# Optimization experiments

Hardware: AMD Instinct MI355X
Metric: run time of the kernel (lower is better)

## Reference

```python
import jax, jax.numpy as jnp
import numpy as np

A, B, I, H, O = 400, 64, 50, 192, 3   # num_agents, batch, input_dim, hidden_dim, output_dim
ADIM, NH = 128, 8                      # attention_dim, num_heads
HD = ADIM // NH
SCALE = HD ** -0.5
EPS = 1e-5


def _ln(x, g, b):
    mu = jnp.mean(x, -1, keepdims=True)
    v = jnp.mean((x - mu) ** 2, -1, keepdims=True)
    return (x - mu) * jax.lax.rsqrt(v + EPS) * g + b


def setup_inputs() -> dict:
    key = jax.random.key(0)
    ks = jax.random.split(key, 12)
    s = 0.05
    n = lambda k, shape: (jax.random.normal(k, shape, jnp.float32) * s)
    return {
        'x': jax.random.normal(ks[0], (B, I), jnp.float32),
        'ln_in_g': jnp.ones((A, I), jnp.float32), 'ln_in_b': jnp.zeros((A, I), jnp.float32),
        'W1': n(ks[1], (A, I, H)), 'b1': jnp.zeros((A, H), jnp.float32),
        'Ws1': n(ks[2], (A, I, H)), 'bs1': jnp.zeros((A, H), jnp.float32),
        'W2': n(ks[3], (A, H, H)), 'b2': jnp.zeros((A, H), jnp.float32),
        'Ws2': n(ks[4], (A, H, H)), 'bs2': jnp.zeros((A, H), jnp.float32),
        'W3': n(ks[5], (A, H, H)), 'b3': jnp.zeros((A, H), jnp.float32),
        'ln_h_g': jnp.ones((A, H), jnp.float32), 'ln_h_b': jnp.zeros((A, H), jnp.float32),
        'Wout': n(ks[6], (A, H, O)), 'bout': jnp.zeros((A, O), jnp.float32),
        'aln_g': jnp.ones((H,), jnp.float32), 'aln_b': jnp.zeros((H,), jnp.float32),
        'Wq': n(ks[7], (H, ADIM)), 'bq': jnp.zeros((ADIM,), jnp.float32),
        'Wk': n(ks[8], (H, ADIM)), 'bk': jnp.zeros((ADIM,), jnp.float32),
        'Wv': n(ks[9], (H, ADIM)), 'bv': jnp.zeros((ADIM,), jnp.float32),
        'Wo': n(ks[10], (ADIM, H)), 'bo': jnp.zeros((H,), jnp.float32),
    }


def _forward(x, ln_in_g, ln_in_b, W1, b1, Ws1, bs1, W2, b2, Ws2, bs2, W3, b3,
             ln_h_g, ln_h_b, Wout, bout, aln_g, aln_b, Wq, bq, Wk, bk, Wv, bv, Wo, bo):
    gelu = lambda t: jax.nn.gelu(t, approximate=False)  # torch F.gelu default = exact erf
    # per-agent input LayerNorm (shared stats, per-agent affine) -> [A, B, I]
    xn = _ln(x[None, :, :], ln_in_g[:, None, :], ln_in_b[:, None, :])
    # agent MLPs as batched GEMMs over agent axis
    h1 = gelu(jnp.einsum('abi,aih->abh', xn, W1) + b1[:, None, :]) \
         + jnp.einsum('abi,aih->abh', xn, Ws1) + bs1[:, None, :]
    h2 = gelu(jnp.einsum('abh,ahk->abk', h1, W2) + b2[:, None, :]) \
         + jnp.einsum('abh,ahk->abk', h1, Ws2) + bs2[:, None, :]
    h3 = _ln(h2 + jnp.einsum('abh,ahk->abk', h2, W3) + b3[:, None, :],
             ln_h_g[:, None, :], ln_h_b[:, None, :])  # [A, B, H]
    # cross-SREK attention across the agent axis
    y = _ln(h3, aln_g, aln_b)
    q = (y @ Wq + bq).reshape(A, B, NH, HD).transpose(1, 2, 0, 3)  # [B, NH, A, HD]
    k = (y @ Wk + bk).reshape(A, B, NH, HD).transpose(1, 2, 0, 3)
    v = (y @ Wv + bv).reshape(A, B, NH, HD).transpose(1, 2, 0, 3)
    attn = jax.nn.softmax(jnp.einsum('bhad,bhcd->bhac', q, k) * SCALE, axis=-1)
    o = jnp.einsum('bhac,bhcd->bhad', attn, v).transpose(2, 0, 1, 3).reshape(A, B, ADIM)
    attended = h3 + (o @ Wo + bo)  # residual (dropout off in eval)
    # per-agent output heads -> [A, B, O]
    logits = jnp.einsum('abh,aho->abo', attended, Wout) + bout[:, None, :]
    return logits


def reference(x, ln_in_g, ln_in_b, W1, b1, Ws1, bs1, W2, b2, Ws2, bs2, W3, b3,
              ln_h_g, ln_h_b, Wout, bout, aln_g, aln_b, Wq, bq, Wk, bk, Wv, bv, Wo, bo):
    return _forward(x, ln_in_g, ln_in_b, W1, b1, Ws1, bs1, W2, b2, Ws2, bs2, W3, b3,
                    ln_h_g, ln_h_b, Wout, bout, aln_g, aln_b, Wq, bq, Wk, bk, Wv, bv, Wo, bo)
```

## Files before the change

### kernel.cpp

```cpp
#include <hip/hip_runtime.h>
#include <math.h>

#define AGENTS 400
#define BATCH  64
#define IDIM   50
#define HDIM   192
#define ODIM   3
#define ADIMM  128
#define NHEADS 8
#define HEADD  16
#define LN_EPS 1e-5f

#define PA   200
#define POUT 136

typedef __bf16 bf16x8 __attribute__((ext_vector_type(8)));
typedef float  f32x4  __attribute__((ext_vector_type(4)));

__device__ __forceinline__ float gelu_exact(float x) {
    return 0.5f * x * (1.0f + erff(x * 0.70710678118654752f));
}

__device__ __forceinline__ unsigned pack_bf16x2(float a, float b) {
    unsigned short ua = __builtin_bit_cast(unsigned short, (__bf16)a);
    unsigned short ub = __builtin_bit_cast(unsigned short, (__bf16)b);
    return (unsigned)ua | ((unsigned)ub << 16);
}

template<int NC, int KD, int NT, int NRG, int LDW, int PITCH>
__device__ __forceinline__ void gemm_bpass(f32x4 (&acc)[NRG][NT],
                                           const float* const* wptr,
                                           const __bf16* Asrc, int lane)
{
    const int r = lane & 15, g = lane >> 4;
    float buf[2][NT * 8];

    #pragma unroll
    for (int t = 0; t < NT; t++)
        #pragma unroll
        for (int j = 0; j < 8; j++) {
            int k = g * 8 + j;
            buf[0][t * 8 + j] = (k < KD) ? wptr[t][k * LDW + r] : 0.f;
        }

    #pragma unroll
    for (int c = 0; c < NC; c++) {
        const int cur = c & 1, nxt = cur ^ 1;
        if (c + 1 < NC) {
            #pragma unroll
            for (int t = 0; t < NT; t++)
                #pragma unroll
                for (int j = 0; j < 8; j++) {
                    int k = (c + 1) * 32 + g * 8 + j;
                    buf[nxt][t * 8 + j] = (k < KD) ? wptr[t][k * LDW + r] : 0.f;
                }
        }
        bf16x8 bfr[NT];
        #pragma unroll
        for (int t = 0; t < NT; t++)
            #pragma unroll
            for (int j = 0; j < 8; j++)
                bfr[t][j] = (__bf16)buf[cur][t * 8 + j];
        #pragma unroll
        for (int rg = 0; rg < NRG; rg++) {
            bf16x8 af = *(const bf16x8*)&Asrc[(16 * rg + r) * PITCH + c * 32 + g * 8];
            #pragma unroll
            for (int t = 0; t < NT; t++)
                acc[rg][t] = __builtin_amdgcn_mfma_f32_16x16x32_bf16(af, bfr[t], acc[rg][t], 0, 0, 0);
        }
    }
}

__global__ __launch_bounds__(512, 4) void mlp_kernel(
    const float* __restrict__ x,
    const float* __restrict__ ln_in_g, const float* __restrict__ ln_in_b,
    const float* __restrict__ W1, const float* __restrict__ b1,
    const float* __restrict__ Ws1, const float* __restrict__ bs1,
    const float* __restrict__ W2, const float* __restrict__ b2,
    const float* __restrict__ Ws2, const float* __restrict__ bs2,
    const float* __restrict__ W3, const float* __restrict__ b3,
    const float* __restrict__ ln_h_g, const float* __restrict__ ln_h_b,
    float* __restrict__ h3out)
{
    const int a    = blockIdx.x;
    const int tid  = threadIdx.x;
    const int wave = tid >> 6, lane = tid & 63;
    const int r = lane & 15, g = lane >> 4;
    const int cg = wave & 3, mh = wave >> 2;
    const int n0 = 48 * cg;
    const __bf16* Aw;

    __shared__ __align__(16) __bf16 As[64 * PA];
    __shared__ float mu_s[64], rs_s[64];
    Aw = As + 32 * mh * PA;

    {
        int rr = tid >> 3, l = tid & 7;
        float s = 0.f, ss = 0.f;
        for (int k = l; k < IDIM; k += 8) { float v = x[rr * IDIM + k]; s += v; ss += v * v; }
        #pragma unroll
        for (int off = 4; off; off >>= 1) {
            s  += __shfl_down(s,  off, 8);
            ss += __shfl_down(ss, off, 8);
        }
        if (l == 0) {
            float mu = s * (1.0f / IDIM);
            float var = ss * (1.0f / IDIM) - mu * mu;
            mu_s[rr] = mu;
            rs_s[rr] = rsqrtf(var + LN_EPS);
        }
    }
    __syncthreads();
    for (int sidx = tid; sidx < 64 * 64; sidx += 512) {
        int rr = sidx >> 6, k = sidx & 63;
        float v = 0.f;
        if (k < IDIM)
            v = (x[rr * IDIM + k] - mu_s[rr]) * rs_s[rr] * ln_in_g[a * IDIM + k] + ln_in_b[a * IDIM + k];
        As[rr * PA + k] = (__bf16)v;
    }
    __syncthreads();

    {
        const float* W1p  = W1  + (size_t)a * IDIM * HDIM;
        const float* Ws1p = Ws1 + (size_t)a * IDIM * HDIM;
        const float* wA[3] = { W1p + n0,  W1p + n0 + 16,  W1p + n0 + 32 };
        const float* wB[3] = { Ws1p + n0, Ws1p + n0 + 16, Ws1p + n0 + 32 };
        f32x4 acc1[2][3];
        #pragma unroll
        for (int i = 0; i < 2; i++)
            #pragma unroll
            for (int t = 0; t < 3; t++) acc1[i][t] = (f32x4)0.f;
        gemm_bpass<2, IDIM, 3, 2, HDIM, PA>(acc1, wA, Aw, lane);
        f32x4 acc2[2][3];
        #pragma unroll
        for (int i = 0; i < 2; i++)
            #pragma unroll
            for (int t = 0; t < 3; t++) acc2[i][t] = (f32x4)0.f;
        gemm_bpass<2, IDIM, 3, 2, HDIM, PA>(acc2, wB, Aw, lane);
        __syncthreads();
        #pragma unroll
        for (int t = 0; t < 3; t++) {
            int col = n0 + 16 * t + r;
            float bb  = b1[a * HDIM + col];
            float bbs = bs1[a * HDIM + col];
            #pragma unroll
            for (int rg = 0; rg < 2; rg++)
                #pragma unroll
                for (int i = 0; i < 4; i++) {
                    int row = 32 * mh + 16 * rg + 4 * g + i;
                    float v = gelu_exact(acc1[rg][t][i] + bb) + acc2[rg][t][i] + bbs;
                    As[row * PA + col] = (__bf16)v;
                }
        }
        __syncthreads();
    }

    {
        const float* W2p  = W2  + (size_t)a * HDIM * HDIM;
        const float* Ws2p = Ws2 + (size_t)a * HDIM * HDIM;
        const float* wA[3] = { W2p + n0,  W2p + n0 + 16,  W2p + n0 + 32 };
        const float* wB[3] = { Ws2p + n0, Ws2p + n0 + 16, Ws2p + n0 + 32 };
        f32x4 acc1[2][3];
        #pragma unroll
        for (int i = 0; i < 2; i++)
            #pragma unroll
            for (int t = 0; t < 3; t++) acc1[i][t] = (f32x4)0.f;
        gemm_bpass<6, HDIM, 3, 2, HDIM, PA>(acc1, wA, Aw, lane);
        f32x4 acc2[2][3];
        #pragma unroll
        for (int i = 0; i < 2; i++)
            #pragma unroll
            for (int t = 0; t < 3; t++) acc2[i][t] = (f32x4)0.f;
        gemm_bpass<6, HDIM, 3, 2, HDIM, PA>(acc2, wB, Aw, lane);
        __syncthreads();
        #pragma unroll
        for (int t = 0; t < 3; t++) {
            int col = n0 + 16 * t + r;
            float bb  = b2[a * HDIM + col];
            float bbs = bs2[a * HDIM + col];
            #pragma unroll
            for (int rg = 0; rg < 2; rg++)
                #pragma unroll
                for (int i = 0; i < 4; i++) {
                    int row = 32 * mh + 16 * rg + 4 * g + i;
                    float v = gelu_exact(acc1[rg][t][i] + bb) + acc2[rg][t][i] + bbs;
                    As[row * PA + col] = (__bf16)v;
                }
        }
        __syncthreads();
    }

    {
        const float* W3p = W3 + (size_t)a * HDIM * HDIM;
        const float* wA[3] = { W3p + n0, W3p + n0 + 16, W3p + n0 + 32 };
        f32x4 acc[2][3];
        #pragma unroll
        for (int i = 0; i < 2; i++)
            #pragma unroll
            for (int t = 0; t < 3; t++) acc[i][t] = (f32x4)0.f;
        gemm_bpass<6, HDIM, 3, 2, HDIM, PA>(acc, wA, Aw, lane);
        __syncthreads();
        #pragma unroll
        for (int t = 0; t < 3; t++) {
            int col = n0 + 16 * t + r;
            float bb = b3[a * HDIM + col];
            #pragma unroll
            for (int rg = 0; rg < 2; rg++)
                #pragma unroll
                for (int i = 0; i < 4; i++) {
                    int row = 32 * mh + 16 * rg + 4 * g + i;
                    float v = (float)As[row * PA + col] + acc[rg][t][i] + bb;
                    As[row * PA + col] = (__bf16)v;
                }
        }
        __syncthreads();
    }

    {
        int rr = tid >> 3, l = tid & 7;
        float s = 0.f, ss = 0.f;
        for (int k = l; k < HDIM; k += 8) { float v = (float)As[rr * PA + k]; s += v; ss += v * v; }
        #pragma unroll
        for (int off = 4; off; off >>= 1) {
            s  += __shfl_down(s,  off, 8);
            ss += __shfl_down(ss, off, 8);
        }
        if (l == 0) {
            float mu = s * (1.0f / HDIM);
            float var = ss * (1.0f / HDIM) - mu * mu;
            mu_s[rr] = mu;
            rs_s[rr] = rsqrtf(var + LN_EPS);
        }
    }
    __syncthreads();
    for (int sidx = tid; sidx < 64 * HDIM; sidx += 512) {
        int rr = sidx / HDIM, c = sidx - rr * HDIM;
        float v = ((float)As[rr * PA + c] - mu_s[rr]) * rs_s[rr] * ln_h_g[a * HDIM + c] + ln_h_b[a * HDIM + c];
        h3out[((size_t)a * BATCH + rr) * HDIM + c] = v;
    }
}

__global__ __launch_bounds__(512, 4) void qkv_kernel(
    const float* __restrict__ h3,
    const float* __restrict__ aln_g, const float* __restrict__ aln_b,
    const float* __restrict__ Wq, const float* __restrict__ bq,
    const float* __restrict__ Wk, const float* __restrict__ bk,
    const float* __restrict__ Wv, const float* __restrict__ bv,
    float* __restrict__ qT, float* __restrict__ kT, float* __restrict__ vT)
{
    const int a    = blockIdx.x;
    const int tid  = threadIdx.x;
    const int wave = tid >> 6, lane = tid & 63;
    const int r = lane & 15, g = lane >> 4;
    const int cg = wave & 3, mh = wave >> 2;

    __shared__ __align__(16) __bf16 ys[64 * PA];
    __shared__ float mu_s[64], rs_s[64];
    const __bf16* Aw = ys + 32 * mh * PA;

    {
        int rr = tid >> 3, l = tid & 7;
        const float* hp = h3 + ((size_t)a * BATCH + rr) * HDIM;
        float s = 0.f, ss = 0.f;
        for (int k = l; k < HDIM; k += 8) { float v = hp[k]; s += v; ss += v * v; }
        #pragma unroll
        for (int off = 4; off; off >>= 1) {
            s  += __shfl_down(s,  off, 8);
            ss += __shfl_down(ss, off, 8);
        }
        if (l == 0) {
            float mu = s * (1.0f / HDIM);
            float var = ss * (1.0f / HDIM) - mu * mu;
            mu_s[rr] = mu;
            rs_s[rr] = rsqrtf(var + LN_EPS);
        }
    }
    __syncthreads();
    for (int sidx = tid; sidx < 64 * HDIM; sidx += 512) {
        int rr = sidx / HDIM, c = sidx - rr * HDIM;
        float v = (h3[((size_t)a * BATCH + rr) * HDIM + c] - mu_s[rr]) * rs_s[rr] * aln_g[c] + aln_b[c];
        ys[rr * PA + c] = (__bf16)v;
    }
    __syncthreads();

    #pragma unroll
    for (int p = 0; p < 2; p++) {
        const int nb = 192 * p + 48 * cg;
        const float* wA[3];
        #pragma unroll
        for (int t = 0; t < 3; t++) {
            int nt = nb + 16 * t;
            const float* base = (nt < 128) ? Wq : (nt < 256) ? Wk : Wv;
            wA[t] = base + (nt & 127);
        }
        f32x4 acc[2][3];
        #pragma unroll
        for (int i = 0; i < 2; i++)
            #pragma unroll
            for (int t = 0; t < 3; t++) acc[i][t] = (f32x4)0.f;
        gemm_bpass<6, HDIM, 3, 2, ADIMM, PA>(acc, wA, Aw, lane);

        #pragma unroll
        for (int t = 0; t < 3; t++) {
            int n = nb + 16 * t + r;
            int which = n >> 7, cc = n & 127, hh = cc >> 4, dd = cc & 15;
            const float* bp = (which == 0) ? bq : (which == 1) ? bk : bv;
            float* op = (which == 0) ? qT : (which == 1) ? kT : vT;
            float bb = bp[cc];
            #pragma unroll
            for (int rg = 0; rg < 2; rg++)
                #pragma unroll
                for (int i = 0; i < 4; i++) {
                    int brow = 32 * mh + 16 * rg + 4 * g + i;
                    op[(((size_t)brow * NHEADS + hh) * AGENTS + a) * HEADD + dd] = acc[rg][t][i] + bb;
                }
        }
    }
}

#define PKA 24
#define PVA 408
#define PPA 232

__global__ __launch_bounds__(256, 2) void attn_kernel(
    const float* __restrict__ qT, const float* __restrict__ kT,
    const float* __restrict__ vT, float* __restrict__ oT)
{
    const int bh   = blockIdx.x;
    const int b    = bh >> 3, h = bh & 7;
    const int tid  = threadIdx.x;
    const int wave = tid >> 6, lane = tid & 63;
    const int r = lane & 15, g = lane >> 4;

    __shared__ __align__(16) __bf16 Ks[AGENTS * PKA];
    __shared__ __align__(16) __bf16 Vt[16 * PVA];
    __shared__ __align__(16) __bf16 Ps[4][16 * PPA];

    const float* kp = kT + (size_t)bh * AGENTS * HEADD;
    const float* vp = vT + (size_t)bh * AGENTS * HEADD;
    for (int idx = tid; idx < AGENTS * HEADD; idx += 256) {
        int a_ = idx >> 4, d = idx & 15;
        Ks[a_ * PKA + d] = (__bf16)kp[idx];
        Vt[d * PVA + a_] = (__bf16)vp[idx];
    }
    __bf16* Pw = Ps[wave];
    for (int z = lane; z < 16 * 16; z += 64)
        Pw[(z >> 4) * PPA + 208 + (z & 15)] = (__bf16)0.f;
    __syncthreads();

    for (int mt = wave; mt < 25; mt += 4) {
        const int m0 = mt * 16;

        bf16x8 aq;
        if (g < 2) {
            const float* qp = qT + ((size_t)bh * AGENTS + m0 + r) * HEADD + g * 8;
            #pragma unroll
            for (int j = 0; j < 8; j++) aq[j] = (__bf16)(qp[j] * 0.25f);
        } else {
            #pragma unroll
            for (int j = 0; j < 8; j++) aq[j] = (__bf16)0.f;
        }

        f32x4 sacc[25];
        #pragma unroll
        for (int t = 0; t < 25; t++) {
            bf16x8 bk_ = *(const bf16x8*)&Ks[(t * 16 + r) * PKA + (g & 1) * 8];
            sacc[t] = __builtin_amdgcn_mfma_f32_16x16x32_bf16(aq, bk_, (f32x4)0.f, 0, 0, 0);
        }

        float lv[4];
        #pragma unroll
        for (int i = 0; i < 4; i++) {
            float m_ = sacc[0][i];
            #pragma unroll
            for (int t = 1; t < 25; t++) m_ = fmaxf(m_, sacc[t][i]);
            #pragma unroll
            for (int off = 8; off; off >>= 1) m_ = fmaxf(m_, __shfl_xor(m_, off, 16));
            float l_ = 0.f;
            #pragma unroll
            for (int t = 0; t < 25; t++) {
                float p = __expf(sacc[t][i] - m_);
                sacc[t][i] = p;
                l_ += p;
            }
            #pragma unroll
            for (int off = 8; off; off >>= 1) l_ += __shfl_xor(l_, off, 16);
            lv[i] = l_;
        }

        f32x4 oacc = (f32x4)0.f;

        #pragma unroll
        for (int t = 0; t < 13; t++)
            #pragma unroll
            for (int i = 0; i < 4; i++)
                Pw[(g * 4 + i) * PPA + t * 16 + r] = (__bf16)sacc[t][i];
        __asm__ volatile("s_waitcnt lgkmcnt(0)" ::: "memory");
        #pragma unroll
        for (int c = 0; c < 7; c++) {
            bf16x8 ap  = *(const bf16x8*)&Pw[r * PPA + c * 32 + g * 8];
            bf16x8 bv_ = *(const bf16x8*)&Vt[r * PVA + c * 32 + g * 8];
            oacc = __builtin_amdgcn_mfma_f32_16x16x32_bf16(ap, bv_, oacc, 0, 0, 0);
        }

        for (int z = lane; z < 16 * 16; z += 64)
            Pw[(z >> 4) * PPA + 192 + (z & 15)] = (__bf16)0.f;
        #pragma unroll
        for (int t = 13; t < 25; t++)
            #pragma unroll
            for (int i = 0; i < 4; i++)
                Pw[(g * 4 + i) * PPA + (t - 13) * 16 + r] = (__bf16)sacc[t][i];
        __asm__ volatile("s_waitcnt lgkmcnt(0)" ::: "memory");
        #pragma unroll
        for (int c = 0; c < 6; c++) {
            bf16x8 ap  = *(const bf16x8*)&Pw[r * PPA + c * 32 + g * 8];
            bf16x8 bv_ = *(const bf16x8*)&Vt[r * PVA + 208 + c * 32 + g * 8];
            oacc = __builtin_amdgcn_mfma_f32_16x16x32_bf16(ap, bv_, oacc, 0, 0, 0);
        }

        #pragma unroll
        for (int i = 0; i < 4; i++)
            oT[((size_t)(m0 + g * 4 + i) * BATCH + b) * ADIMM + h * HEADD + r] = oacc[i] / lv[i];
    }
}

__global__ __launch_bounds__(256, 2) void out_kernel(
    const float* __restrict__ h3, const float* __restrict__ oT,
    const float* __restrict__ Wo, const float* __restrict__ bo,
    const float* __restrict__ Wout, const float* __restrict__ bout,
    float* __restrict__ out)
{
    const int a    = blockIdx.x;
    const int tid  = threadIdx.x;
    const int wave = tid >> 6, lane = tid & 63;
    const int r = lane & 15, g = lane >> 4;
    const int n0 = 48 * wave;

    __shared__ __align__(16) __bf16 os[64 * POUT];
    __shared__ __align__(16) __bf16 att[64 * PA];

    for (int idx = tid; idx < 64 * 32; idx += 256) {
        int bb = idx >> 5, q = idx & 31;
        float4 v = ((const float4*)(oT + ((size_t)a * BATCH + bb) * ADIMM))[q];
        unsigned u0 = pack_bf16x2(v.x, v.y);
        unsigned u1 = pack_bf16x2(v.z, v.w);
        *(uint2*)&os[bb * POUT + q * 4] = make_uint2(u0, u1);
    }
    __syncthreads();

    {
        const float* wA[3] = { Wo + n0, Wo + n0 + 16, Wo + n0 + 32 };
        f32x4 acc[4][3];
        #pragma unroll
        for (int i = 0; i < 4; i++)
            #pragma unroll
            for (int t = 0; t < 3; t++) acc[i][t] = (f32x4)0.f;
        gemm_bpass<4, ADIMM, 3, 4, HDIM, POUT>(acc, wA, os, lane);
        #pragma unroll
        for (int t = 0; t < 3; t++) {
            int col = n0 + 16 * t + r;
            float bb = bo[col];
            #pragma unroll
            for (int rg = 0; rg < 4; rg++)
                #pragma unroll
                for (int i = 0; i < 4; i++) {
                    int row = 16 * rg + 4 * g + i;
                    float v = h3[((size_t)a * BATCH + row) * HDIM + col] + acc[rg][t][i] + bb;
                    att[row * PA + col] = (__bf16)v;
                }
        }
    }
    __syncthreads();

    {
        const float* Wp = Wout + (size_t)a * HDIM * ODIM;
        float wb[48];
        #pragma unroll
        for (int c = 0; c < 6; c++)
            #pragma unroll
            for (int j = 0; j < 8; j++) {
                int k = c * 32 + g * 8 + j;
                wb[c * 8 + j] = (r < ODIM) ? Wp[k * ODIM + r] : 0.f;
            }
        f32x4 oacc = (f32x4)0.f;
        #pragma unroll
        for (int c = 0; c < 6; c++) {
            bf16x8 bf;
            #pragma unroll
            for (int j = 0; j < 8; j++) bf[j] = (__bf16)wb[c * 8 + j];
            bf16x8 af = *(const bf16x8*)&att[(16 * wave + r) * PA + c * 32 + g * 8];
            oacc = __builtin_amdgcn_mfma_f32_16x16x32_bf16(af, bf, oacc, 0, 0, 0);
        }
        if (r < ODIM) {
            float bb = bout[a * ODIM + r];
            #pragma unroll
            for (int i = 0; i < 4; i++) {
                int row = 16 * wave + 4 * g + i;
                out[((size_t)a * BATCH + row) * ODIM + r] = oacc[i] + bb;
            }
        }
    }
}

extern "C" void kernel_launch(void* const* d_in, const int* in_sizes, int n_in,
                              void* d_out, int out_size, void* d_ws, size_t ws_size,
                              hipStream_t stream)
{
    const float* x       = (const float*)d_in[0];
    const float* ln_in_g = (const float*)d_in[1];
    const float* ln_in_b = (const float*)d_in[2];
    const float* W1      = (const float*)d_in[3];
    const float* b1      = (const float*)d_in[4];
    const float* Ws1     = (const float*)d_in[5];
    const float* bs1     = (const float*)d_in[6];
    const float* W2      = (const float*)d_in[7];
    const float* b2      = (const float*)d_in[8];
    const float* Ws2     = (const float*)d_in[9];
    const float* bs2     = (const float*)d_in[10];
    const float* W3      = (const float*)d_in[11];
    const float* b3      = (const float*)d_in[12];
    const float* ln_h_g  = (const float*)d_in[13];
    const float* ln_h_b  = (const float*)d_in[14];
    const float* Wout    = (const float*)d_in[15];
    const float* bout    = (const float*)d_in[16];
    const float* aln_g   = (const float*)d_in[17];
    const float* aln_b   = (const float*)d_in[18];
    const float* Wq      = (const float*)d_in[19];
    const float* bq      = (const float*)d_in[20];
    const float* Wk      = (const float*)d_in[21];
    const float* bk      = (const float*)d_in[22];
    const float* Wv      = (const float*)d_in[23];
    const float* bv      = (const float*)d_in[24];
    const float* Wo      = (const float*)d_in[25];
    const float* bo      = (const float*)d_in[26];
    float* out = (float*)d_out;

    float* ws = (float*)d_ws;
    const size_t H3_SZ = (size_t)AGENTS * BATCH * HDIM;
    const size_t QT_SZ = (size_t)BATCH * NHEADS * AGENTS * HEADD;
    float* h3 = ws;
    float* qT = h3 + H3_SZ;
    float* kT = qT + QT_SZ;
    float* vT = kT + QT_SZ;
    float* oT = vT + QT_SZ;

    mlp_kernel<<<AGENTS, 512, 0, stream>>>(x, ln_in_g, ln_in_b,
                                           W1, b1, Ws1, bs1, W2, b2, Ws2, bs2,
                                           W3, b3, ln_h_g, ln_h_b, h3);
    qkv_kernel<<<AGENTS, 512, 0, stream>>>(h3, aln_g, aln_b,
                                           Wq, bq, Wk, bk, Wv, bv, qT, kT, vT);
    attn_kernel<<<BATCH * NHEADS, 256, 0, stream>>>(qT, kT, vT, oT);
    out_kernel<<<AGENTS, 256, 0, stream>>>(h3, oT, Wo, bo, Wout, bout, out);
}
```

Baseline: 435.3 us.

## Halve MLP/QKV block size so each wave covers all 64 rows, reusing weight fragments

The MLP and QKV kernels drop from 512 to 256 threads per block. Each wave now computes all 64 batch rows for its 48 columns, so every weight fragment loaded from global memory feeds four MFMA row groups instead of two. This halves redundant weight loads, which matters because the per-agent weights are streamed from global memory. A second LDS buffer (Bs) ping-pongs with As so the two GEMMs of each layer can write results without the intermediate barrier; the cost is more accumulator registers per wave, fewer waves per block, and more LDS use.

```diff
diff --git a/kernel.cpp b/kernel.cpp
--- a/kernel.cpp
+++ b/kernel.cpp
@@ -71,7 +71,7 @@
     }
 }
 
-__global__ __launch_bounds__(512, 4) void mlp_kernel(
+__global__ __launch_bounds__(256, 3) void mlp_kernel(
     const float* __restrict__ x,
     const float* __restrict__ ln_in_g, const float* __restrict__ ln_in_b,
     const float* __restrict__ W1, const float* __restrict__ b1,
@@ -86,23 +86,18 @@
     const int tid  = threadIdx.x;
     const int wave = tid >> 6, lane = tid & 63;
     const int r = lane & 15, g = lane >> 4;
-    const int cg = wave & 3, mh = wave >> 2;
-    const int n0 = 48 * cg;
-    const __bf16* Aw;
+    const int n0 = 48 * wave;
 
     __shared__ __align__(16) __bf16 As[64 * PA];
+    __shared__ __align__(16) __bf16 Bs[64 * PA];
     __shared__ float mu_s[64], rs_s[64];
-    Aw = As + 32 * mh * PA;
-
-    {
-        int rr = tid >> 3, l = tid & 7;
+
+    {
+        int rr = tid >> 2, l = tid & 3;
         float s = 0.f, ss = 0.f;
-        for (int k = l; k < IDIM; k += 8) { float v = x[rr * IDIM + k]; s += v; ss += v * v; }
-        #pragma unroll
-        for (int off = 4; off; off >>= 1) {
-            s  += __shfl_down(s,  off, 8);
-            ss += __shfl_down(ss, off, 8);
-        }
+        for (int k = l; k < IDIM; k += 4) { float v = x[rr * IDIM + k]; s += v; ss += v * v; }
+        s  += __shfl_down(s, 2, 4);  s  += __shfl_down(s, 1, 4);
+        ss += __shfl_down(ss, 2, 4); ss += __shfl_down(ss, 1, 4);
         if (l == 0) {
             float mu = s * (1.0f / IDIM);
             float var = ss * (1.0f / IDIM) - mu * mu;
@@ -111,7 +106,7 @@
         }
     }
     __syncthreads();
-    for (int sidx = tid; sidx < 64 * 64; sidx += 512) {
+    for (int sidx = tid; sidx < 64 * 64; sidx += 256) {
         int rr = sidx >> 6, k = sidx & 63;
         float v = 0.f;
         if (k < IDIM)
@@ -123,34 +118,47 @@
     {
         const float* W1p  = W1  + (size_t)a * IDIM * HDIM;
         const float* Ws1p = Ws1 + (size_t)a * IDIM * HDIM;
-        const float* wA[3] = { W1p + n0,  W1p + n0 + 16,  W1p + n0 + 32 };
-        const float* wB[3] = { Ws1p + n0, Ws1p + n0 + 16, Ws1p + n0 + 32 };
-        f32x4 acc1[2][3];
-        #pragma unroll
-        for (int i = 0; i < 2; i++)
-            #pragma unroll
-            for (int t = 0; t < 3; t++) acc1[i][t] = (f32x4)0.f;
-        gemm_bpass<2, IDIM, 3, 2, HDIM, PA>(acc1, wA, Aw, lane);
-        f32x4 acc2[2][3];
-        #pragma unroll
-        for (int i = 0; i < 2; i++)
-            #pragma unroll
-            for (int t = 0; t < 3; t++) acc2[i][t] = (f32x4)0.f;
-        gemm_bpass<2, IDIM, 3, 2, HDIM, PA>(acc2, wB, Aw, lane);
-        __syncthreads();
-        #pragma unroll
-        for (int t = 0; t < 3; t++) {
-            int col = n0 + 16 * t + r;
-            float bb  = b1[a * HDIM + col];
-            float bbs = bs1[a * HDIM + col];
-            #pragma unroll
-            for (int rg = 0; rg < 2; rg++)
-                #pragma unroll
-                for (int i = 0; i < 4; i++) {
-                    int row = 32 * mh + 16 * rg + 4 * g + i;
-                    float v = gelu_exact(acc1[rg][t][i] + bb) + acc2[rg][t][i] + bbs;
-                    As[row * PA + col] = (__bf16)v;
-                }
+        {
+            const float* wA[3] = { W1p + n0, W1p + n0 + 16, W1p + n0 + 32 };
+            f32x4 acc[4][3];
+            #pragma unroll
+            for (int i = 0; i < 4; i++)
+                #pragma unroll
+                for (int t = 0; t < 3; t++) acc[i][t] = (f32x4)0.f;
+            gemm_bpass<2, IDIM, 3, 4, HDIM, PA>(acc, wA, As, lane);
+            #pragma unroll
+            for (int t = 0; t < 3; t++) {
+                int col = n0 + 16 * t + r;
+                float bb  = b1[a * HDIM + col];
+                float bbs = bs1[a * HDIM + col];
+                #pragma unroll
+                for (int rg = 0; rg < 4; rg++)
+                    #pragma unroll
+                    for (int i = 0; i < 4; i++) {
+                        int row = 16 * rg + 4 * g + i;
+                        Bs[row * PA + col] = (__bf16)(gelu_exact(acc[rg][t][i] + bb) + bbs);
+                    }
+            }
+        }
+        {
+            const float* wB[3] = { Ws1p + n0, Ws1p + n0 + 16, Ws1p + n0 + 32 };
+            f32x4 acc[4][3];
+            #pragma unroll
+            for (int i = 0; i < 4; i++)
+                #pragma unroll
+                for (int t = 0; t < 3; t++) acc[i][t] = (f32x4)0.f;
+            gemm_bpass<2, IDIM, 3, 4, HDIM, PA>(acc, wB, As, lane);
+            #pragma unroll
+            for (int t = 0; t < 3; t++) {
+                int col = n0 + 16 * t + r;
+                #pragma unroll
+                for (int rg = 0; rg < 4; rg++)
+                    #pragma unroll
+                    for (int i = 0; i < 4; i++) {
+                        int row = 16 * rg + 4 * g + i;
+                        Bs[row * PA + col] = (__bf16)((float)Bs[row * PA + col] + acc[rg][t][i]);
+                    }
+            }
         }
         __syncthreads();
     }
@@ -158,34 +166,47 @@
     {
         const float* W2p  = W2  + (size_t)a * HDIM * HDIM;
         const float* Ws2p = Ws2 + (size_t)a * HDIM * HDIM;
-        const float* wA[3] = { W2p + n0,  W2p + n0 + 16,  W2p + n0 + 32 };
-        const float* wB[3] = { Ws2p + n0, Ws2p + n0 + 16, Ws2p + n0 + 32 };
-        f32x4 acc1[2][3];
-        #pragma unroll
-        for (int i = 0; i < 2; i++)
-            #pragma unroll
-            for (int t = 0; t < 3; t++) acc1[i][t] = (f32x4)0.f;
-        gemm_bpass<6, HDIM, 3, 2, HDIM, PA>(acc1, wA, Aw, lane);
-        f32x4 acc2[2][3];
-        #pragma unroll
-        for (int i = 0; i < 2; i++)
-            #pragma unroll
-            for (int t = 0; t < 3; t++) acc2[i][t] = (f32x4)0.f;
-        gemm_bpass<6, HDIM, 3, 2, HDIM, PA>(acc2, wB, Aw, lane);
-        __syncthreads();
-        #pragma unroll
-        for (int t = 0; t < 3; t++) {
-            int col = n0 + 16 * t + r;
-            float bb  = b2[a * HDIM + col];
-            float bbs = bs2[a * HDIM + col];
-            #pragma unroll
-            for (int rg = 0; rg < 2; rg++)
-                #pragma unroll
-                for (int i = 0; i < 4; i++) {
-                    int row = 32 * mh + 16 * rg + 4 * g + i;
-                    float v = gelu_exact(acc1[rg][t][i] + bb) + acc2[rg][t][i] + bbs;
-                    As[row * PA + col] = (__bf16)v;
-                }
+        {
+            const float* wA[3] = { W2p + n0, W2p + n0 + 16, W2p + n0 + 32 };
+            f32x4 acc[4][3];
+            #pragma unroll
+            for (int i = 0; i < 4; i++)
+                #pragma unroll
+                for (int t = 0; t < 3; t++) acc[i][t] = (f32x4)0.f;
+            gemm_bpass<6, HDIM, 3, 4, HDIM, PA>(acc, wA, Bs, lane);
+            #pragma unroll
+            for (int t = 0; t < 3; t++) {
+                int col = n0 + 16 * t + r;
+                float bb  = b2[a * HDIM + col];
+                float bbs = bs2[a * HDIM + col];
+                #pragma unroll
+                for (int rg = 0; rg < 4; rg++)
+                    #pragma unroll
+                    for (int i = 0; i < 4; i++) {
+                        int row = 16 * rg + 4 * g + i;
+                        As[row * PA + col] = (__bf16)(gelu_exact(acc[rg][t][i] + bb) + bbs);
+                    }
+            }
+        }
+        {
+            const float* wB[3] = { Ws2p + n0, Ws2p + n0 + 16, Ws2p + n0 + 32 };
+            f32x4 acc[4][3];
+            #pragma unroll
+            for (int i = 0; i < 4; i++)
+                #pragma unroll
+                for (int t = 0; t < 3; t++) acc[i][t] = (f32x4)0.f;
+            gemm_bpass<6, HDIM, 3, 4, HDIM, PA>(acc, wB, Bs, lane);
+            #pragma unroll
+            for (int t = 0; t < 3; t++) {
+                int col = n0 + 16 * t + r;
+                #pragma unroll
+                for (int rg = 0; rg < 4; rg++)
+                    #pragma unroll
+                    for (int i = 0; i < 4; i++) {
+                        int row = 16 * rg + 4 * g + i;
+                        As[row * PA + col] = (__bf16)((float)As[row * PA + col] + acc[rg][t][i]);
+                    }
+            }
         }
         __syncthreads();
     }
@@ -193,38 +214,33 @@
     {
         const float* W3p = W3 + (size_t)a * HDIM * HDIM;
         const float* wA[3] = { W3p + n0, W3p + n0 + 16, W3p + n0 + 32 };
-        f32x4 acc[2][3];
-        #pragma unroll
-        for (int i = 0; i < 2; i++)
+        f32x4 acc[4][3];
+        #pragma unroll
+        for (int i = 0; i < 4; i++)
             #pragma unroll
             for (int t = 0; t < 3; t++) acc[i][t] = (f32x4)0.f;
-        gemm_bpass<6, HDIM, 3, 2, HDIM, PA>(acc, wA, Aw, lane);
-        __syncthreads();
+        gemm_bpass<6, HDIM, 3, 4, HDIM, PA>(acc, wA, As, lane);
         #pragma unroll
         for (int t = 0; t < 3; t++) {
             int col = n0 + 16 * t + r;
             float bb = b3[a * HDIM + col];
             #pragma unroll
-            for (int rg = 0; rg < 2; rg++)
+            for (int rg = 0; rg < 4; rg++)
                 #pragma unroll
                 for (int i = 0; i < 4; i++) {
-                    int row = 32 * mh + 16 * rg + 4 * g + i;
-                    float v = (float)As[row * PA + col] + acc[rg][t][i] + bb;
-                    As[row * PA + col] = (__bf16)v;
+                    int row = 16 * rg + 4 * g + i;
+                    Bs[row * PA + col] = (__bf16)((float)As[row * PA + col] + acc[rg][t][i] + bb);
                 }
         }
         __syncthreads();
     }
 
     {
-        int rr = tid >> 3, l = tid & 7;
+        int rr = tid >> 2, l = tid & 3;
         float s = 0.f, ss = 0.f;
-        for (int k = l; k < HDIM; k += 8) { float v = (float)As[rr * PA + k]; s += v; ss += v * v; }
-        #pragma unroll
-        for (int off = 4; off; off >>= 1) {
-            s  += __shfl_down(s,  off, 8);
-            ss += __shfl_down(ss, off, 8);
-        }
+        for (int k = l; k < HDIM; k += 4) { float v = (float)Bs[rr * PA + k]; s += v; ss += v * v; }
+        s  += __shfl_down(s, 2, 4);  s  += __shfl_down(s, 1, 4);
+        ss += __shfl_down(ss, 2, 4); ss += __shfl_down(ss, 1, 4);
         if (l == 0) {
             float mu = s * (1.0f / HDIM);
             float var = ss * (1.0f / HDIM) - mu * mu;
@@ -233,14 +249,14 @@
         }
     }
     __syncthreads();
-    for (int sidx = tid; sidx < 64 * HDIM; sidx += 512) {
+    for (int sidx = tid; sidx < 64 * HDIM; sidx += 256) {
         int rr = sidx / HDIM, c = sidx - rr * HDIM;
-        float v = ((float)As[rr * PA + c] - mu_s[rr]) * rs_s[rr] * ln_h_g[a * HDIM + c] + ln_h_b[a * HDIM + c];
+        float v = ((float)Bs[rr * PA + c] - mu_s[rr]) * rs_s[rr] * ln_h_g[a * HDIM + c] + ln_h_b[a * HDIM + c];
         h3out[((size_t)a * BATCH + rr) * HDIM + c] = v;
     }
 }
 
-__global__ __launch_bounds__(512, 4) void qkv_kernel(
+__global__ __launch_bounds__(256, 3) void qkv_kernel(
     const float* __restrict__ h3,
     const float* __restrict__ aln_g, const float* __restrict__ aln_b,
     const float* __restrict__ Wq, const float* __restrict__ bq,
@@ -252,22 +268,17 @@
     const int tid  = threadIdx.x;
     const int wave = tid >> 6, lane = tid & 63;
     const int r = lane & 15, g = lane >> 4;
-    const int cg = wave & 3, mh = wave >> 2;
 
     __shared__ __align__(16) __bf16 ys[64 * PA];
     __shared__ float mu_s[64], rs_s[64];
-    const __bf16* Aw = ys + 32 * mh * PA;
-
-    {
-        int rr = tid >> 3, l = tid & 7;
+
+    {
+        int rr = tid >> 2, l = tid & 3;
         const float* hp = h3 + ((size_t)a * BATCH + rr) * HDIM;
         float s = 0.f, ss = 0.f;
-        for (int k = l; k < HDIM; k += 8) { float v = hp[k]; s += v; ss += v * v; }
-        #pragma unroll
-        for (int off = 4; off; off >>= 1) {
-            s  += __shfl_down(s,  off, 8);
-            ss += __shfl_down(ss, off, 8);
-        }
+        for (int k = l; k < HDIM; k += 4) { float v = hp[k]; s += v; ss += v * v; }
+        s  += __shfl_down(s, 2, 4);  s  += __shfl_down(s, 1, 4);
+        ss += __shfl_down(ss, 2, 4); ss += __shfl_down(ss, 1, 4);
         if (l == 0) {
             float mu = s * (1.0f / HDIM);
             float var = ss * (1.0f / HDIM) - mu * mu;
@@ -276,7 +287,7 @@
         }
     }
     __syncthreads();
-    for (int sidx = tid; sidx < 64 * HDIM; sidx += 512) {
+    for (int sidx = tid; sidx < 64 * HDIM; sidx += 256) {
         int rr = sidx / HDIM, c = sidx - rr * HDIM;
         float v = (h3[((size_t)a * BATCH + rr) * HDIM + c] - mu_s[rr]) * rs_s[rr] * aln_g[c] + aln_b[c];
         ys[rr * PA + c] = (__bf16)v;
@@ -285,7 +296,7 @@
 
     #pragma unroll
     for (int p = 0; p < 2; p++) {
-        const int nb = 192 * p + 48 * cg;
+        const int nb = 192 * p + 48 * wave;
         const float* wA[3];
         #pragma unroll
         for (int t = 0; t < 3; t++) {
@@ -293,12 +304,12 @@
             const float* base = (nt < 128) ? Wq : (nt < 256) ? Wk : Wv;
             wA[t] = base + (nt & 127);
         }
-        f32x4 acc[2][3];
-        #pragma unroll
-        for (int i = 0; i < 2; i++)
+        f32x4 acc[4][3];
+        #pragma unroll
+        for (int i = 0; i < 4; i++)
             #pragma unroll
             for (int t = 0; t < 3; t++) acc[i][t] = (f32x4)0.f;
-        gemm_bpass<6, HDIM, 3, 2, ADIMM, PA>(acc, wA, Aw, lane);
+        gemm_bpass<6, HDIM, 3, 4, ADIMM, PA>(acc, wA, ys, lane);
 
         #pragma unroll
         for (int t = 0; t < 3; t++) {
@@ -308,10 +319,10 @@
             float* op = (which == 0) ? qT : (which == 1) ? kT : vT;
             float bb = bp[cc];
             #pragma unroll
-            for (int rg = 0; rg < 2; rg++)
+            for (int rg = 0; rg < 4; rg++)
                 #pragma unroll
                 for (int i = 0; i < 4; i++) {
-                    int brow = 32 * mh + 16 * rg + 4 * g + i;
+                    int brow = 16 * rg + 4 * g + i;
                     op[(((size_t)brow * NHEADS + hh) * AGENTS + a) * HEADD + dd] = acc[rg][t][i] + bb;
                 }
         }
@@ -424,7 +435,7 @@
     }
 }
 
-__global__ __launch_bounds__(256, 2) void out_kernel(
+__global__ __launch_bounds__(256, 3) void out_kernel(
     const float* __restrict__ h3, const float* __restrict__ oT,
     const float* __restrict__ Wo, const float* __restrict__ bo,
     const float* __restrict__ Wout, const float* __restrict__ bout,
@@ -544,10 +555,10 @@
     float* vT = kT + QT_SZ;
     float* oT = vT + QT_SZ;
 
-    mlp_kernel<<<AGENTS, 512, 0, stream>>>(x, ln_in_g, ln_in_b,
+    mlp_kernel<<<AGENTS, 256, 0, stream>>>(x, ln_in_g, ln_in_b,
                                            W1, b1, Ws1, bs1, W2, b2, Ws2, bs2,
                                            W3, b3, ln_h_g, ln_h_b, h3);
-    qkv_kernel<<<AGENTS, 512, 0, stream>>>(h3, aln_g, aln_b,
+    qkv_kernel<<<AGENTS, 256, 0, stream>>>(h3, aln_g, aln_b,
                                            Wq, bq, Wk, bk, Wv, bv, qT, kT, vT);
     attn_kernel<<<BATCH * NHEADS, 256, 0, stream>>>(qT, kT, vT, oT);
     out_kernel<<<AGENTS, 256, 0, stream>>>(h3, oT, Wo, bo, Wout, bout, out);
```

Result: slower. 464.6 us (+6.7%).
